# Kernel tuning notes

Measured on AMD Instinct MI355X. Metric: run time of the kernel, lower is better.

The kernel has to match this reference:

```python
import jax, jax.numpy as jnp
import numpy as np

B_, C_, NH_, WS_, HID_ = 8, 512, 16, 7, 2048
HH, WW = 56, 56


def _rel_pos_index(ws):
    coords = np.stack(np.meshgrid(np.arange(ws), np.arange(ws), indexing='ij'))  # (2,ws,ws)
    cf = coords.reshape(2, -1)
    rc = (cf[:, :, None] - cf[:, None, :]).transpose(1, 2, 0)  # (ws2,ws2,2)
    rc[..., 0] += ws - 1
    rc[..., 1] += ws - 1
    rc[..., 0] *= 2 * ws - 1
    return jnp.asarray(rc.sum(-1).reshape(-1))  # (ws2*ws2,)


def _ln(x, g, b, eps):
    mu = x.mean(-1, keepdims=True)
    var = ((x - mu) ** 2).mean(-1, keepdims=True)
    return (x - mu) * jax.lax.rsqrt(var + eps) * g + b


def setup_inputs() -> dict:
    key = jax.random.key(0)
    ks = jax.random.split(key, 8)
    s = lambda k, shape: (jax.random.normal(k, shape, jnp.float32) * 0.02)
    return {
        'x': jax.random.normal(ks[0], (B_, HH * WW, C_), jnp.float32),
        'H': HH, 'W': WW,
        'norm1_g': jnp.ones((C_,), jnp.float32), 'norm1_b': jnp.zeros((C_,), jnp.float32),
        'norm2_g': jnp.ones((C_,), jnp.float32), 'norm2_b': jnp.zeros((C_,), jnp.float32),
        'qkv_w': s(ks[1], (3 * C_, C_)), 'qkv_b': jnp.zeros((3 * C_,), jnp.float32),
        'rpb': s(ks[2], ((2 * WS_ - 1) ** 2, NH_)),
        'fc1_w': s(ks[3], (HID_, C_)), 'fc1_b': jnp.zeros((HID_,), jnp.float32),
        'dw_w': s(ks[4], (HID_, 1, 3, 3)), 'dw_b': jnp.zeros((HID_,), jnp.float32),
        'fc2_w': s(ks[5], (C_, HID_)), 'fc2_b': jnp.zeros((C_,), jnp.float32),
    }


def reference(x, H, W, norm1_g, norm1_b, norm2_g, norm2_b, qkv_w, qkv_b, rpb,
              fc1_w, fc1_b, dw_w, dw_b, fc2_w, fc2_b):
    B, N, C = x.shape
    ws, nh = WS_, NH_
    hd = C // nh
    scale = hd ** -0.5
    ws2 = ws * ws
    nHw, nWw = H // ws, W // ws

    # ---- norm1 + WaveAttention (windowed attention w/ relative position bias) ----
    h = _ln(x, norm1_g, norm1_b, 1e-5)
    qkv = h @ qkv_w.T + qkv_b                                   # [B,N,3C]
    # window partition: [B, nH, ws, nW, ws, 3, nh, hd] -> [3, B*nH*nW, nh, ws2, hd]
    qkv = qkv.reshape(B, nHw, ws, nWw, ws, 3, nh, hd)
    qkv = qkv.transpose(5, 0, 1, 3, 6, 2, 4, 7).reshape(3, B * nHw * nWw, nh, ws2, hd)
    q, k, v = qkv[0], qkv[1], qkv[2]

    attn = jnp.einsum('wnid,wnjd->wnij', q, k) * scale          # [Bw,nh,ws2,ws2]
    bias = rpb[_rel_pos_index(ws)].reshape(ws2, ws2, nh).transpose(2, 0, 1)
    attn = jax.nn.softmax(attn + bias[None], axis=-1)
    out = jnp.einsum('wnij,wnjd->wnid', attn, v)                # [Bw,nh,ws2,hd]
    # window reverse
    out = out.transpose(0, 2, 1, 3).reshape(B, nHw, nWw, ws, ws, C)
    out = out.transpose(0, 1, 3, 2, 4, 5).reshape(B, N, C)
    x = x + out

    # ---- norm2 + PVT2FFN (fc1 -> depthwise 3x3 conv -> GELU -> fc2) ----
    h2 = _ln(x, norm2_g, norm2_b, 1e-5)
    h2 = h2 @ fc1_w.T + fc1_b                                   # [B,N,HID]
    img = h2.reshape(B, H, W, HID_).transpose(0, 3, 1, 2)       # [B,HID,H,W]
    img = jax.lax.conv_general_dilated(img, dw_w, (1, 1), 'SAME',
                                       feature_group_count=HID_)
    img = img + dw_b[None, :, None, None]
    h2 = img.reshape(B, HID_, N).transpose(0, 2, 1)
    h2 = jax.nn.gelu(h2, approximate=False)
    h2 = h2 @ fc2_w.T + fc2_b
    return x + h2
```

## Files before the change

### kernel.cpp

```cpp
#include <hip/hip_runtime.h>
#include <hip/hip_bf16.h>

typedef unsigned short u16;
typedef unsigned int u32;
typedef __attribute__((ext_vector_type(8))) short bf16x8_t;
typedef __attribute__((ext_vector_type(4))) float f32x4_t;
typedef __attribute__((ext_vector_type(8))) u16 u16x8;
typedef __attribute__((ext_vector_type(4))) u32 u32x4;

constexpr int B_  = 8;
constexpr int C_  = 512;
constexpr int NH_ = 16;
constexpr int HID_= 2048;
constexpr int Hh  = 56, Ww = 56;
constexpr int N_  = Hh * Ww;
constexpr int M_  = B_ * N_;

__device__ __forceinline__ u16 f2bf(float f) {
    u32 u = __float_as_uint(f);
    u32 r = (u + 0x7fffu + ((u >> 16) & 1u)) >> 16;
    return (u16)r;
}
__device__ __forceinline__ float bf2f(u16 v) {
    return __uint_as_float(((u32)v) << 16);
}

__device__ __forceinline__ void bar_raw() {
    __asm__ __volatile__("s_barrier" ::: "memory");
}

typedef const void __attribute__((address_space(1))) gvoid_t;
typedef void __attribute__((address_space(3))) lvoid_t;
__device__ __forceinline__ void gload16(const u16* g, u16* l) {
    __builtin_amdgcn_global_load_lds((gvoid_t*)g, (lvoid_t*)l, 16, 0, 0);
}

__global__ void cvt_w(const float* __restrict__ qkvw, const float* __restrict__ fc1w,
                      const float* __restrict__ fc2w, u16* __restrict__ oq,
                      u16* __restrict__ o1, u16* __restrict__ o2) {
    int i = blockIdx.x * 256 + threadIdx.x;
    if (i < 3 * C_ * C_) oq[i] = f2bf(qkvw[i]);
    if (i < HID_ * C_) { o1[i] = f2bf(fc1w[i]); o2[i] = f2bf(fc2w[i]); }
}

__global__ __launch_bounds__(256) void ln_kernel(const float* __restrict__ x,
        const float* __restrict__ g, const float* __restrict__ b, u16* __restrict__ out) {
    int lane = threadIdx.x & 63, wv = threadIdx.x >> 6;
    size_t row = (size_t)blockIdx.x * 4 + wv;
    const float4* xr = (const float4*)(x + row * C_);
    float4 a = xr[lane * 2], c = xr[lane * 2 + 1];
    float s  = a.x + a.y + a.z + a.w + c.x + c.y + c.z + c.w;
    float ss = a.x*a.x + a.y*a.y + a.z*a.z + a.w*a.w + c.x*c.x + c.y*c.y + c.z*c.z + c.w*c.w;
    #pragma unroll
    for (int off = 1; off < 64; off <<= 1) {
        s  += __shfl_xor(s, off);
        ss += __shfl_xor(ss, off);
    }
    float mean = s * (1.0f / C_);
    float var  = ss * (1.0f / C_) - mean * mean;
    float rstd = rsqrtf(var + 1e-5f);
    const float4* g4 = (const float4*)g;
    const float4* b4 = (const float4*)b;
    float4 g0 = g4[lane*2], g1 = g4[lane*2+1], b0 = b4[lane*2], b1 = b4[lane*2+1];
    u16x8 o;
    o[0] = f2bf((a.x - mean) * rstd * g0.x + b0.x);
    o[1] = f2bf((a.y - mean) * rstd * g0.y + b0.y);
    o[2] = f2bf((a.z - mean) * rstd * g0.z + b0.z);
    o[3] = f2bf((a.w - mean) * rstd * g0.w + b0.w);
    o[4] = f2bf((c.x - mean) * rstd * g1.x + b1.x);
    o[5] = f2bf((c.y - mean) * rstd * g1.y + b1.y);
    o[6] = f2bf((c.z - mean) * rstd * g1.z + b1.z);
    o[7] = f2bf((c.w - mean) * rstd * g1.w + b1.w);
    *(u16x8*)&out[row * C_ + lane * 8] = o;
}

template<bool RES, bool OUT_BF16>
__global__ __launch_bounds__(256) void gemm_bt(
        const u16* __restrict__ A, const u16* __restrict__ B,
        const float* __restrict__ bias, const float* __restrict__ res,
        void* __restrict__ Cout, int M, int N, int K,
        int nbm, int nbn, int nGroups) {
    const int id = blockIdx.x;
    const int xcd = id & 7, slot = id >> 3;
    const int j = slot & 3;
    const int gidx = xcd + 8 * (slot >> 2);
    if (gidx >= nGroups) return;
    const int bm = gidx % nbm;
    const int bn = (gidx / nbm) * 4 + j;
    if (bn >= nbn) return;

    __shared__ __align__(16) u16 As[2 * 128 * 32];
    __shared__ __align__(16) u16 Bs[2 * 128 * 32];
    const int tid = threadIdx.x;
    const int lane = tid & 63;
    const int wv = tid >> 6;

    const int r0 = lane >> 2;
    const int gcb = ((lane & 3) ^ ((lane >> 3) & 3));

    const u16* aBase = A + (size_t)(bm * 128) * K;
    const u16* bBase = B + (size_t)(bn * 128) * K;

    f32x4_t acc[4][4];
    f32x4_t zero = {0.f, 0.f, 0.f, 0.f};
    #pragma unroll
    for (int i = 0; i < 4; i++)
        #pragma unroll
        for (int jj = 0; jj < 4; jj++) acc[i][jj] = zero;

    const int mo = (wv >> 1) * 64, no = (wv & 1) * 64;
    const int fr = lane & 15;
    const int g4 = lane >> 4;
    const int kkey = (fr >> 1) & 3;
    const int pos = (g4 ^ kkey) * 8;

    for (int k0 = 0; k0 < K; k0 += 64) {
        #pragma unroll
        for (int p = 0; p < 2; p++)
            #pragma unroll
            for (int jj = 0; jj < 2; jj++) {
                const size_t go = (size_t)((wv + jj * 4) * 16 + r0) * K
                                + (size_t)(k0 + p * 32 + gcb * 8);
                gload16(aBase + go, &As[p * 4096 + (wv + jj * 4) * 512]);
                gload16(bBase + go, &Bs[p * 4096 + (wv + jj * 4) * 512]);
            }
        __asm__ __volatile__("s_waitcnt vmcnt(0)" ::: "memory");
        bar_raw();

        #pragma unroll
        for (int ks = 0; ks < 2; ks++) {
            bf16x8_t af[4], bfr[4];
            #pragma unroll
            for (int mt = 0; mt < 4; mt++)
                af[mt] = *(const bf16x8_t*)&As[ks * 4096 + (mo + mt * 16 + fr) * 32 + pos];
            #pragma unroll
            for (int nt = 0; nt < 4; nt++)
                bfr[nt] = *(const bf16x8_t*)&Bs[ks * 4096 + (no + nt * 16 + fr) * 32 + pos];
            #pragma unroll
            for (int mt = 0; mt < 4; mt++)
                #pragma unroll
                for (int nt = 0; nt < 4; nt++)
                    acc[mt][nt] = __builtin_amdgcn_mfma_f32_16x16x32_bf16(af[mt], bfr[nt], acc[mt][nt], 0, 0, 0);
        }
        bar_raw();
    }

    #pragma unroll
    for (int mt = 0; mt < 4; mt++) {
        #pragma unroll
        for (int r = 0; r < 4; r++) {
            int row = bm * 128 + mo + mt * 16 + (lane >> 4) * 4 + r;
            #pragma unroll
            for (int nt = 0; nt < 4; nt++) {
                int col = bn * 128 + no + nt * 16 + (lane & 15);
                float v = acc[mt][nt][r] + bias[col];
                if constexpr (RES) v += res[(size_t)row * N + col];
                if constexpr (OUT_BF16) ((u16*)Cout)[(size_t)row * N + col] = f2bf(v);
                else ((float*)Cout)[(size_t)row * N + col] = v;
            }
        }
    }
}

constexpr int QS = 40;
constexpr int VS = 72;
constexpr int PS = 72;

__global__ __launch_bounds__(256) void attn_kernel(
        const u16* __restrict__ qkv, const float* __restrict__ rpb,
        u16* __restrict__ aout) {
    __shared__ __align__(16) u16 q_s[64 * QS];
    __shared__ __align__(16) u16 k_s[64 * QS];
    __shared__ __align__(16) u16 vT_s[32 * VS];
    __shared__ __align__(16) u16 p_s[64 * PS];
    const int tid = threadIdx.x, lane = tid & 63, wv = tid >> 6;
    const int wh = blockIdx.x;
    const int head = wh & 15, w = wh >> 4;
    const int b = w >> 6, win = w & 63, bh = win >> 3, bw = win & 7;

    {
        int i = tid >> 2, dc = (tid & 3) * 8;
        if (i < 49) {
            int n = (bh * 7 + i / 7) * Ww + (bw * 7 + i % 7);
            const u16* base = qkv + ((size_t)(b * N_ + n)) * (3 * C_) + head * 32 + dc;
            *(u16x8*)&q_s[i * QS + dc] = *(const u16x8*)(base);
            *(u16x8*)&k_s[i * QS + dc] = *(const u16x8*)(base + C_);
        } else {
            u16x8 z = {0,0,0,0,0,0,0,0};
            *(u16x8*)&q_s[i * QS + dc] = z;
            *(u16x8*)&k_s[i * QS + dc] = z;
        }
    }
    for (int f = tid; f < 64 * 32; f += 256) {
        int i = f >> 5, d = f & 31;
        u16 val = 0;
        if (i < 49) {
            int n = (bh * 7 + i / 7) * Ww + (bw * 7 + i % 7);
            val = qkv[((size_t)(b * N_ + n)) * (3 * C_) + 2 * C_ + head * 32 + d];
        }
        vT_s[d * VS + i] = val;
    }
    __syncthreads();

    f32x4_t zero = {0.f, 0.f, 0.f, 0.f};
    f32x4_t s[4];
    bf16x8_t aq = *(const bf16x8_t*)&q_s[(wv * 16 + (lane & 15)) * QS + (lane >> 4) * 8];
    #pragma unroll
    for (int nt = 0; nt < 4; nt++) {
        bf16x8_t bk = *(const bf16x8_t*)&k_s[(nt * 16 + (lane & 15)) * QS + (lane >> 4) * 8];
        s[nt] = __builtin_amdgcn_mfma_f32_16x16x32_bf16(aq, bk, zero, 0, 0, 0);
    }

    const float scale = 0.17677669529663687f;
    #pragma unroll
    for (int r = 0; r < 4; r++) {
        int row = wv * 16 + (lane >> 4) * 4 + r;
        int qy = row / 7, qx = row - qy * 7;
        float pv[4];
        float m = -1e30f;
        #pragma unroll
        for (int nt = 0; nt < 4; nt++) {
            int col = nt * 16 + (lane & 15);
            float bias;
            if (row < 49 && col < 49) {
                int ky = col / 7, kx = col - ky * 7;
                bias = rpb[((qy - ky + 6) * 13 + (qx - kx + 6)) * NH_ + head];
            } else bias = -1e30f;
            float v = s[nt][r] * scale + bias;
            pv[nt] = v;
            m = fmaxf(m, v);
        }
        #pragma unroll
        for (int off = 1; off < 16; off <<= 1) m = fmaxf(m, __shfl_xor(m, off));
        float sum = 0.f;
        #pragma unroll
        for (int nt = 0; nt < 4; nt++) { pv[nt] = __expf(pv[nt] - m); sum += pv[nt]; }
        #pragma unroll
        for (int off = 1; off < 16; off <<= 1) sum += __shfl_xor(sum, off);
        float inv = 1.0f / sum;
        #pragma unroll
        for (int nt = 0; nt < 4; nt++)
            p_s[row * PS + nt * 16 + (lane & 15)] = f2bf(pv[nt] * inv);
    }
    __syncthreads();

    f32x4_t o[2] = {zero, zero};
    #pragma unroll
    for (int kt = 0; kt < 2; kt++) {
        bf16x8_t ap = *(const bf16x8_t*)&p_s[(wv * 16 + (lane & 15)) * PS + kt * 32 + (lane >> 4) * 8];
        #pragma unroll
        for (int nt = 0; nt < 2; nt++) {
            bf16x8_t bv = *(const bf16x8_t*)&vT_s[(nt * 16 + (lane & 15)) * VS + kt * 32 + (lane >> 4) * 8];
            o[nt] = __builtin_amdgcn_mfma_f32_16x16x32_bf16(ap, bv, o[nt], 0, 0, 0);
        }
    }
    u16* obase = aout + ((size_t)(w * 16 + head)) * 49 * 32;
    #pragma unroll
    for (int nt = 0; nt < 2; nt++) {
        #pragma unroll
        for (int r = 0; r < 4; r++) {
            int row = wv * 16 + (lane >> 4) * 4 + r;
            if (row < 49)
                obase[row * 32 + nt * 16 + (lane & 15)] = f2bf(o[nt][r]);
        }
    }
}

__global__ __launch_bounds__(256) void wrev_ln(const float* __restrict__ x,
        const u16* __restrict__ aout, const float* __restrict__ g,
        const float* __restrict__ bt, float* __restrict__ x2, u16* __restrict__ h) {
    int lane = threadIdx.x & 63, wvv = threadIdx.x >> 6;
    int m = blockIdx.x * 4 + wvv;
    int b = m / N_, n = m - b * N_;
    int iy = n / Ww, ix = n - iy * Ww;
    int w = b * 64 + (iy / 7) * 8 + (ix / 7);
    int pos = (iy % 7) * 7 + (ix % 7);
    int head = lane >> 2, d0 = (lane & 3) * 8;
    u16x8 ao = *(const u16x8*)&aout[(((size_t)w * 16 + head) * 49 + pos) * 32 + d0];
    const float4* xr = (const float4*)(x + (size_t)m * C_ + lane * 8);
    float4 a = xr[0], c = xr[1];
    float v[8];
    v[0] = a.x + bf2f(ao[0]); v[1] = a.y + bf2f(ao[1]);
    v[2] = a.z + bf2f(ao[2]); v[3] = a.w + bf2f(ao[3]);
    v[4] = c.x + bf2f(ao[4]); v[5] = c.y + bf2f(ao[5]);
    v[6] = c.z + bf2f(ao[6]); v[7] = c.w + bf2f(ao[7]);
    float s = 0.f, ss = 0.f;
    #pragma unroll
    for (int jj = 0; jj < 8; jj++) { s += v[jj]; ss += v[jj] * v[jj]; }
    #pragma unroll
    for (int off = 1; off < 64; off <<= 1) {
        s  += __shfl_xor(s, off);
        ss += __shfl_xor(ss, off);
    }
    float mean = s * (1.0f / C_);
    float var  = ss * (1.0f / C_) - mean * mean;
    float rstd = rsqrtf(var + 1e-5f);
    float4 o0 = {v[0], v[1], v[2], v[3]}, o1 = {v[4], v[5], v[6], v[7]};
    float4* x2r = (float4*)(x2 + (size_t)m * C_ + lane * 8);
    x2r[0] = o0; x2r[1] = o1;
    const float4* g4 = (const float4*)(g + lane * 8);
    const float4* b4 = (const float4*)(bt + lane * 8);
    float4 g0 = g4[0], g1 = g4[1], bb0 = b4[0], bb1 = b4[1];
    u16x8 o;
    o[0] = f2bf((v[0] - mean) * rstd * g0.x + bb0.x);
    o[1] = f2bf((v[1] - mean) * rstd * g0.y + bb0.y);
    o[2] = f2bf((v[2] - mean) * rstd * g0.z + bb0.z);
    o[3] = f2bf((v[3] - mean) * rstd * g0.w + bb0.w);
    o[4] = f2bf((v[4] - mean) * rstd * g1.x + bb1.x);
    o[5] = f2bf((v[5] - mean) * rstd * g1.y + bb1.y);
    o[6] = f2bf((v[6] - mean) * rstd * g1.z + bb1.z);
    o[7] = f2bf((v[7] - mean) * rstd * g1.w + bb1.w);
    *(u16x8*)&h[(size_t)m * C_ + lane * 8] = o;
}

__global__ __launch_bounds__(256) void dwconv_gelu(const u16* __restrict__ in,
        const float* __restrict__ w, const float* __restrict__ bias, u16* __restrict__ out) {
    const int t = threadIdx.x;
    const int blk = blockIdx.x;
    const int xq = blk & 3;
    const int byp = blk >> 2;
    const int yp = byp % 28;
    const int b = byp / 28;
    const int y0 = yp * 2;
    const int c0 = t * 8;

    float wr[9][8];
    #pragma unroll
    for (int k = 0; k < 9; k++)
        #pragma unroll
        for (int j = 0; j < 8; j++) wr[k][j] = w[(c0 + j) * 9 + k];
    float bs[8];
    #pragma unroll
    for (int j = 0; j < 8; j++) bs[j] = bias[c0 + j];

    u16x8 zerov = {0,0,0,0,0,0,0,0};
    auto ldcol = [&](int xx, u16x8* col) {
        #pragma unroll
        for (int dy = 0; dy < 4; dy++) {
            int yy = y0 + dy - 1;
            bool ok = (yy >= 0 && yy < Hh && xx >= 0 && xx < Ww);
            col[dy] = ok ? *(const u16x8*)&in[(((size_t)b * Hh + yy) * Ww + xx) * HID_ + c0] : zerov;
        }
    };

    int xs = xq * 14;
    u16x8 wA[4], wB[4], wC[4];
    ldcol(xs - 1, wA);
    ldcol(xs, wB);
    for (int x = xs; x < xs + 14; x++) {
        ldcol(x + 1, wC);
        float acc0[8], acc1[8];
        #pragma unroll
        for (int j = 0; j < 8; j++) { acc0[j] = bs[j]; acc1[j] = bs[j]; }
        #pragma unroll
        for (int dy = 0; dy < 3; dy++)
            #pragma unroll
            for (int j = 0; j < 8; j++) {
                acc0[j] += bf2f(wA[dy][j]) * wr[dy * 3 + 0][j];
                acc0[j] += bf2f(wB[dy][j]) * wr[dy * 3 + 1][j];
                acc0[j] += bf2f(wC[dy][j]) * wr[dy * 3 + 2][j];
                acc1[j] += bf2f(wA[dy + 1][j]) * wr[dy * 3 + 0][j];
                acc1[j] += bf2f(wB[dy + 1][j]) * wr[dy * 3 + 1][j];
                acc1[j] += bf2f(wC[dy + 1][j]) * wr[dy * 3 + 2][j];
            }
        u16x8 o0, o1;
        #pragma unroll
        for (int j = 0; j < 8; j++) {
            float v0 = acc0[j];
            o0[j] = f2bf(0.5f * v0 * (1.0f + erff(v0 * 0.70710678118654752f)));
            float v1 = acc1[j];
            o1[j] = f2bf(0.5f * v1 * (1.0f + erff(v1 * 0.70710678118654752f)));
        }
        *(u16x8*)&out[(((size_t)b * Hh + y0) * Ww + x) * HID_ + c0] = o0;
        *(u16x8*)&out[(((size_t)b * Hh + y0 + 1) * Ww + x) * HID_ + c0] = o1;
        #pragma unroll
        for (int dy = 0; dy < 4; dy++) { wA[dy] = wB[dy]; wB[dy] = wC[dy]; }
    }
}

extern "C" void kernel_launch(void* const* d_in, const int* in_sizes, int n_in,
                              void* d_out, int out_size, void* d_ws, size_t ws_size,
                              hipStream_t stream) {
    const float* x    = (const float*)d_in[0];
    const float* n1g  = (const float*)d_in[3];
    const float* n1b  = (const float*)d_in[4];
    const float* n2g  = (const float*)d_in[5];
    const float* n2b  = (const float*)d_in[6];
    const float* qkvw = (const float*)d_in[7];
    const float* qkvb = (const float*)d_in[8];
    const float* rpb  = (const float*)d_in[9];
    const float* fc1w = (const float*)d_in[10];
    const float* fc1b = (const float*)d_in[11];
    const float* dww  = (const float*)d_in[12];
    const float* dwb  = (const float*)d_in[13];
    const float* fc2w = (const float*)d_in[14];
    const float* fc2b = (const float*)d_in[15];

    char* ws = (char*)d_ws;
    float* x2  = (float*)(ws);
    u16*   h   = (u16*)(ws + 51380224);
    u16*   qkvo= (u16*)(ws + 77070336);
    u16*   aout= (u16*)(ws + 154140672);
    u16*   f1o = (u16*)(ws + 154140672);
    u16*   cvo = (u16*)(ws + 51380224);
    u16*   wq  = (u16*)(ws + 256901120);
    u16*   w1  = (u16*)(ws + 256901120 + 1572864);
    u16*   w2  = (u16*)(ws + 256901120 + 1572864 + 2097152);

    auto ggrid = [](int nGroups) { return 32 * ((nGroups + 7) / 8); };

    cvt_w<<<dim3(4096), dim3(256), 0, stream>>>(qkvw, fc1w, fc2w, wq, w1, w2);
    ln_kernel<<<dim3(M_ / 4), dim3(256), 0, stream>>>(x, n1g, n1b, h);
    gemm_bt<false, true><<<dim3(ggrid(588)), dim3(256), 0, stream>>>(
        h, wq, qkvb, nullptr, (void*)qkvo, M_, 1536, 512, 196, 12, 588);
    attn_kernel<<<dim3(B_ * 64 * NH_), dim3(256), 0, stream>>>(qkvo, rpb, aout);
    wrev_ln<<<dim3(M_ / 4), dim3(256), 0, stream>>>(x, aout, n2g, n2b, x2, h);
    gemm_bt<false, true><<<dim3(ggrid(784)), dim3(256), 0, stream>>>(
        h, w1, fc1b, nullptr, (void*)f1o, M_, 2048, 512, 196, 16, 784);
    dwconv_gelu<<<dim3(B_ * 28 * 4), dim3(256), 0, stream>>>(f1o, dww, dwb, cvo);
    gemm_bt<true, false><<<dim3(ggrid(196)), dim3(256), 0, stream>>>(
        cvo, w2, fc2b, x2, d_out, M_, 512, 2048, 196, 4, 196);
}
```

Baseline: 542.7 us.

## Replace 128x128 GEMM with 256x256-tile, 8-wave, prefetch-pipelined GEMM

Replaces the 128x128-tile, 4-wave GEMM with a 256x256-tile, 512-thread kernel. It double-buffers LDS (128 KB total) and issues global loads for the next one and two K-steps in the middle of the MFMA phases. This raises reuse per loaded byte and overlaps memory traffic with compute, using s_setprio to favour the MFMA phases. The XCD-aware block-to-tile mapping is also rewritten as a contiguous chunk per XCD. The risk is the fc2 GEMM, which now launches only 196 blocks and so leaves many CUs idle. The large LDS footprint also limits each CU to one block.

```diff
diff --git a/kernel.cpp b/kernel.cpp
--- a/kernel.cpp
+++ b/kernel.cpp
@@ -75,91 +75,133 @@
 }
 
 template<bool RES, bool OUT_BF16>
-__global__ __launch_bounds__(256) void gemm_bt(
+__global__ __launch_bounds__(512) void gemm256(
         const u16* __restrict__ A, const u16* __restrict__ B,
         const float* __restrict__ bias, const float* __restrict__ res,
         void* __restrict__ Cout, int M, int N, int K,
-        int nbm, int nbn, int nGroups) {
+        int nbm, int nbn) {
+    const int nwg = nbm * nbn;
     const int id = blockIdx.x;
-    const int xcd = id & 7, slot = id >> 3;
-    const int j = slot & 3;
-    const int gidx = xcd + 8 * (slot >> 2);
-    if (gidx >= nGroups) return;
-    const int bm = gidx % nbm;
-    const int bn = (gidx / nbm) * 4 + j;
-    if (bn >= nbn) return;
-
-    __shared__ __align__(16) u16 As[2 * 128 * 32];
-    __shared__ __align__(16) u16 Bs[2 * 128 * 32];
+    const int xcd = id & 7, i = id >> 3;
+    const int q = nwg >> 3, r = nwg & 7;
+    const int gidx = (xcd < r ? xcd * (q + 1) : r * (q + 1) + (xcd - r) * q) + i;
+    const int bm = gidx / nbn;
+    const int bn = gidx - bm * nbn;
+
+    __shared__ __align__(16) u16 As[2 * 16384];
+    __shared__ __align__(16) u16 Bs[2 * 16384];
     const int tid = threadIdx.x;
     const int lane = tid & 63;
-    const int wv = tid >> 6;
+    const int w = tid >> 6;
+    const int qr = w >> 1, qc = w & 1;
 
     const int r0 = lane >> 2;
     const int gcb = ((lane & 3) ^ ((lane >> 3) & 3));
-
-    const u16* aBase = A + (size_t)(bm * 128) * K;
-    const u16* bBase = B + (size_t)(bn * 128) * K;
-
-    f32x4_t acc[4][4];
-    f32x4_t zero = {0.f, 0.f, 0.f, 0.f};
-    #pragma unroll
-    for (int i = 0; i < 4; i++)
-        #pragma unroll
-        for (int jj = 0; jj < 4; jj++) acc[i][jj] = zero;
-
-    const int mo = (wv >> 1) * 64, no = (wv & 1) * 64;
     const int fr = lane & 15;
     const int g4 = lane >> 4;
-    const int kkey = (fr >> 1) & 3;
-    const int pos = (g4 ^ kkey) * 8;
-
-    for (int k0 = 0; k0 < K; k0 += 64) {
-        #pragma unroll
-        for (int p = 0; p < 2; p++)
+    const int swz = (g4 ^ ((fr >> 1) & 3)) * 8;
+
+    const u16* aBase = A + (size_t)(bm * 256) * K;
+    const u16* bBase = B + (size_t)(bn * 256) * K;
+
+    f32x4_t acc[2][2][2][4];
+    f32x4_t zero = {0.f, 0.f, 0.f, 0.f};
+    #pragma unroll
+    for (int a0 = 0; a0 < 2; a0++)
+        #pragma unroll
+        for (int b0 = 0; b0 < 2; b0++)
             #pragma unroll
-            for (int jj = 0; jj < 2; jj++) {
-                const size_t go = (size_t)((wv + jj * 4) * 16 + r0) * K
-                                + (size_t)(k0 + p * 32 + gcb * 8);
-                gload16(aBase + go, &As[p * 4096 + (wv + jj * 4) * 512]);
-                gload16(bBase + go, &Bs[p * 4096 + (wv + jj * 4) * 512]);
+            for (int c0 = 0; c0 < 2; c0++)
+                #pragma unroll
+                for (int d0 = 0; d0 < 4; d0++) acc[a0][b0][c0][d0] = zero;
+
+    auto stage = [&](const u16* gb, u16* lb, int u, int hf) {
+        const u16* src = gb + (size_t)(hf * 128 + w * 16 + r0) * K
+                            + (size_t)(u * 64 + gcb * 8);
+        u16* dst = lb + (u & 1) * 16384 + hf * 8192 + w * 512;
+        gload16(src, dst);
+        gload16(src + 32, dst + 4096);
+    };
+
+    const int NT = K >> 6;
+    stage(aBase, As, 0, 0);
+    stage(bBase, Bs, 0, 0);
+    stage(aBase, As, 0, 1);
+    stage(bBase, Bs, 0, 1);
+    stage(bBase, Bs, 1, 0);
+    stage(aBase, As, 1, 0);
+    __asm__ __volatile__("s_waitcnt vmcnt(4)" ::: "memory");
+    bar_raw();
+
+    for (int t = 0; t < NT; t++) {
+        const int bb = (t & 1) * 16384;
+        bf16x8_t bfv[2][4];
+        #pragma unroll
+        for (int pp = 0; pp < 4; pp++) {
+            const int mh = pp & 1, nh = pp >> 1;
+            bf16x8_t af[2][2];
+            #pragma unroll
+            for (int ks = 0; ks < 2; ks++)
+                #pragma unroll
+                for (int mf = 0; mf < 2; mf++)
+                    af[ks][mf] = *(const bf16x8_t*)&As[bb + mh * 8192 + ks * 4096
+                                    + (qr * 2 + mf) * 512 + fr * 32 + swz];
+            if (pp == 0 || pp == 2) {
+                #pragma unroll
+                for (int ks = 0; ks < 2; ks++)
+                    #pragma unroll
+                    for (int nf = 0; nf < 4; nf++)
+                        bfv[ks][nf] = *(const bf16x8_t*)&Bs[bb + nh * 8192 + ks * 4096
+                                        + (qc * 4 + nf) * 512 + fr * 32 + swz];
             }
-        __asm__ __volatile__("s_waitcnt vmcnt(0)" ::: "memory");
-        bar_raw();
-
-        #pragma unroll
-        for (int ks = 0; ks < 2; ks++) {
-            bf16x8_t af[4], bfr[4];
+            if (pp == 0) {
+                if (t + 1 < NT) stage(aBase, As, t + 1, 1);
+            } else if (pp == 1) {
+                if (t + 1 < NT) stage(bBase, Bs, t + 1, 1);
+            } else if (pp == 2) {
+                if (t + 2 < NT) stage(bBase, Bs, t + 2, 0);
+            } else {
+                if (t + 2 < NT) {
+                    stage(aBase, As, t + 2, 0);
+                    __asm__ __volatile__("s_waitcnt vmcnt(4)" ::: "memory");
+                } else if (t + 1 < NT) {
+                    __asm__ __volatile__("s_waitcnt vmcnt(0)" ::: "memory");
+                }
+            }
+            bar_raw();
+            __asm__ __volatile__("s_waitcnt lgkmcnt(0)" ::: "memory");
+            __builtin_amdgcn_s_setprio(1);
             #pragma unroll
-            for (int mt = 0; mt < 4; mt++)
-                af[mt] = *(const bf16x8_t*)&As[ks * 4096 + (mo + mt * 16 + fr) * 32 + pos];
+            for (int mf = 0; mf < 2; mf++)
+                #pragma unroll
+                for (int nf = 0; nf < 4; nf++)
+                    #pragma unroll
+                    for (int ks = 0; ks < 2; ks++)
+                        acc[mh][nh][mf][nf] = __builtin_amdgcn_mfma_f32_16x16x32_bf16(
+                            af[ks][mf], bfv[ks][nf], acc[mh][nh][mf][nf], 0, 0, 0);
+            __builtin_amdgcn_s_setprio(0);
+            bar_raw();
+        }
+    }
+
+    #pragma unroll
+    for (int mh = 0; mh < 2; mh++)
+        #pragma unroll
+        for (int nh = 0; nh < 2; nh++)
             #pragma unroll
-            for (int nt = 0; nt < 4; nt++)
-                bfr[nt] = *(const bf16x8_t*)&Bs[ks * 4096 + (no + nt * 16 + fr) * 32 + pos];
-            #pragma unroll
-            for (int mt = 0; mt < 4; mt++)
+            for (int mf = 0; mf < 2; mf++)
                 #pragma unroll
-                for (int nt = 0; nt < 4; nt++)
-                    acc[mt][nt] = __builtin_amdgcn_mfma_f32_16x16x32_bf16(af[mt], bfr[nt], acc[mt][nt], 0, 0, 0);
-        }
-        bar_raw();
-    }
-
-    #pragma unroll
-    for (int mt = 0; mt < 4; mt++) {
-        #pragma unroll
-        for (int r = 0; r < 4; r++) {
-            int row = bm * 128 + mo + mt * 16 + (lane >> 4) * 4 + r;
-            #pragma unroll
-            for (int nt = 0; nt < 4; nt++) {
-                int col = bn * 128 + no + nt * 16 + (lane & 15);
-                float v = acc[mt][nt][r] + bias[col];
-                if constexpr (RES) v += res[(size_t)row * N + col];
-                if constexpr (OUT_BF16) ((u16*)Cout)[(size_t)row * N + col] = f2bf(v);
-                else ((float*)Cout)[(size_t)row * N + col] = v;
-            }
-        }
-    }
+                for (int rr = 0; rr < 4; rr++) {
+                    int row = bm * 256 + mh * 128 + qr * 32 + mf * 16 + (lane >> 4) * 4 + rr;
+                    #pragma unroll
+                    for (int nf = 0; nf < 4; nf++) {
+                        int col = bn * 256 + nh * 128 + qc * 64 + nf * 16 + (lane & 15);
+                        float v = acc[mh][nh][mf][nf][rr] + bias[col];
+                        if constexpr (RES) v += res[(size_t)row * N + col];
+                        if constexpr (OUT_BF16) ((u16*)Cout)[(size_t)row * N + col] = f2bf(v);
+                        else ((float*)Cout)[(size_t)row * N + col] = v;
+                    }
+                }
 }
 
 constexpr int QS = 40;
@@ -407,17 +449,15 @@
     u16*   w1  = (u16*)(ws + 256901120 + 1572864);
     u16*   w2  = (u16*)(ws + 256901120 + 1572864 + 2097152);
 
-    auto ggrid = [](int nGroups) { return 32 * ((nGroups + 7) / 8); };
-
     cvt_w<<<dim3(4096), dim3(256), 0, stream>>>(qkvw, fc1w, fc2w, wq, w1, w2);
     ln_kernel<<<dim3(M_ / 4), dim3(256), 0, stream>>>(x, n1g, n1b, h);
-    gemm_bt<false, true><<<dim3(ggrid(588)), dim3(256), 0, stream>>>(
-        h, wq, qkvb, nullptr, (void*)qkvo, M_, 1536, 512, 196, 12, 588);
+    gemm256<false, true><<<dim3(588), dim3(512), 0, stream>>>(
+        h, wq, qkvb, nullptr, (void*)qkvo, M_, 1536, 512, 98, 6);
     attn_kernel<<<dim3(B_ * 64 * NH_), dim3(256), 0, stream>>>(qkvo, rpb, aout);
     wrev_ln<<<dim3(M_ / 4), dim3(256), 0, stream>>>(x, aout, n2g, n2b, x2, h);
-    gemm_bt<false, true><<<dim3(ggrid(784)), dim3(256), 0, stream>>>(
-        h, w1, fc1b, nullptr, (void*)f1o, M_, 2048, 512, 196, 16, 784);
+    gemm256<false, true><<<dim3(784), dim3(512), 0, stream>>>(
+        h, w1, fc1b, nullptr, (void*)f1o, M_, 2048, 512, 98, 8);
     dwconv_gelu<<<dim3(B_ * 28 * 4), dim3(256), 0, stream>>>(f1o, dww, dwb, cvo);
-    gemm_bt<true, false><<<dim3(ggrid(196)), dim3(256), 0, stream>>>(
-        cvo, w2, fc2b, x2, d_out, M_, 512, 2048, 196, 4, 196);
-}
+    gemm256<true, false><<<dim3(196), dim3(512), 0, stream>>>(
+        cvo, w2, fc2b, x2, d_out, M_, 512, 2048, 98, 2);
+}
```

Result: faster. 523.6 us (-3.5%).
